# Kernel optimization log

Measured on AMD Instinct MI355X. Metric: run time of the kernel, lower is better.

The kernel has to match this reference:

```python
import jax, jax.numpy as jnp
import numpy as np

F_, H_, W_ = 6, 16, 28          # latent video grid (frames, height, width)
DIM, NH = 1536, 12
HD = DIM // NH                   # 128
L = F_ * H_ * W_                 # 2688 tokens
EPS = 1e-6
BLOCK = 3 * H_ * W_              # block_causal_size = 3*frame_height*frame_width


def setup_inputs() -> dict:
    key = jax.random.key(0)
    ks = jax.random.split(key, 8)
    def lin(k):
        return jax.random.normal(k, (DIM, DIM), jnp.float32) * 0.02
    x = jax.random.normal(ks[0], (1, L, DIM), jnp.float32)
    # RoPE freqs: unit-modulus complex numbers stored as [...,(re,im)]
    ang = jax.random.uniform(ks[1], (1024, HD // 2), jnp.float32, -np.pi, np.pi)
    freqs = jnp.stack([jnp.cos(ang), jnp.sin(ang)], axis=-1)  # [1024, 64, 2]
    return {
        'x': x,
        'seq_lens': jnp.array([L], jnp.int32),
        'grid_sizes': jnp.array([[F_, H_, W_]], jnp.int32),
        'freqs': freqs,
        'Wq': lin(ks[2]), 'bq': jnp.zeros((DIM,), jnp.float32),
        'Wk': lin(ks[3]), 'bk': jnp.zeros((DIM,), jnp.float32),
        'Wv': lin(ks[4]), 'bv': jnp.zeros((DIM,), jnp.float32),
        'Wo': lin(ks[5]), 'bo': jnp.zeros((DIM,), jnp.float32),
        'gq': jnp.ones((DIM,), jnp.float32),
        'gk': jnp.ones((DIM,), jnp.float32),
    }


def _rmsnorm(x, g):
    # WanRMSNorm: x * rsqrt(mean(x^2) + eps) * weight
    return x * jax.lax.rsqrt(jnp.mean(x * x, axis=-1, keepdims=True) + EPS) * g


def _rope_apply(x, F, H, W, freqs, start_frame=0):
    # x: [B, L, n, d]; freqs: [1024, d//2, 2] (re, im). Per-axis split [c0, c3, c3].
    B, Lx, n, d = x.shape
    c = d // 2
    c3 = c // 3
    c0 = c - 2 * c3
    f0 = freqs[start_frame:start_frame + F, :c0]      # [F, c0, 2]
    f1 = freqs[:H, c0:c0 + c3]                        # [H, c3, 2]
    f2 = freqs[:W, c0 + c3:]                          # [W, c3, 2]
    ff = jnp.concatenate([
        jnp.broadcast_to(f0[:, None, None], (F, H, W, c0, 2)),
        jnp.broadcast_to(f1[None, :, None], (F, H, W, c3, 2)),
        jnp.broadcast_to(f2[None, None, :], (F, H, W, c3, 2)),
    ], axis=3).reshape(Lx, 1, c, 2)                   # [L, 1, c, 2]
    xr = x.reshape(B, Lx, n, c, 2)
    xre, xim = xr[..., 0], xr[..., 1]
    fre, fim = ff[None, ..., 0], ff[None, ..., 1]     # broadcast over batch, heads
    ore = xre * fre - xim * fim
    oim = xre * fim + xim * fre
    return jnp.stack([ore, oim], axis=-1).reshape(B, Lx, n, d)


def reference(x, seq_lens, grid_sizes, freqs, Wq, bq, Wk, bk, Wv, bv, Wo, bo, gq, gk):
    b, s = x.shape[:2]
    F = int(grid_sizes[0, 0]); H = int(grid_sizes[0, 1]); W = int(grid_sizes[0, 2])
    q = _rmsnorm(x @ Wq + bq, gq).reshape(b, s, NH, HD)
    k = _rmsnorm(x @ Wk + bk, gk).reshape(b, s, NH, HD)
    v = (x @ Wv + bv).reshape(b, s, NH, HD)
    rq = _rope_apply(q, F, H, W, freqs)
    rk = _rope_apply(k, F, H, W, freqs)
    # block-causal attention: query attends to keys in same-or-earlier 3-frame block
    scores = jnp.einsum('bihd,bjhd->bhij', rq, rk) * (HD ** -0.5)
    blk = jnp.arange(s) // (3 * H * W)
    mask = blk[None, :] <= blk[:, None]               # [s, s]
    scores = jnp.where(mask[None, None], scores, -1e30)
    attn = jax.nn.softmax(scores, axis=-1)
    out = jnp.einsum('bhij,bjhd->bihd', attn, v).reshape(b, s, DIM)
    return out @ Wo + bo
```

## Files before the change

kernel.cpp:

```cpp
#include <hip/hip_runtime.h>

#define L_SEQ 2688
#define DIM   1536
#define NH    12
#define HD    128
#define BLK_TOK 1344
#define HW_   448
#define W_    28

typedef unsigned short u16;
typedef unsigned int   u32;
typedef __attribute__((ext_vector_type(4))) float f32x4;
typedef __attribute__((ext_vector_type(8))) short s16x8;

__device__ __forceinline__ u16 f2b(float f) {
    u32 u = __builtin_bit_cast(u32, f);
    return (u16)((u + 0x7FFFu + ((u >> 16) & 1u)) >> 16);
}
__device__ __forceinline__ float b2f(u16 b) {
    return __builtin_bit_cast(float, (u32)b << 16);
}

__global__ __launch_bounds__(256) void k_cvt_x(const float* __restrict__ x,
                                               u16* __restrict__ xb, int n4) {
    int i = blockIdx.x * 256 + threadIdx.x;
    int stride = gridDim.x * 256;
    for (; i < n4; i += stride) {
        float4 v = ((const float4*)x)[i];
        ushort4 o;
        o.x = f2b(v.x); o.y = f2b(v.y); o.z = f2b(v.z); o.w = f2b(v.w);
        ((ushort4*)xb)[i] = o;
    }
}

__global__ __launch_bounds__(256) void k_trans_w(const float* __restrict__ w0,
                                                 const float* __restrict__ w1,
                                                 const float* __restrict__ w2,
                                                 const float* __restrict__ w3,
                                                 u16* __restrict__ wt_all) {
    const float* w = blockIdx.z == 0 ? w0 : blockIdx.z == 1 ? w1 : blockIdx.z == 2 ? w2 : w3;
    u16* wt = wt_all + (size_t)blockIdx.z * DIM * DIM;
    __shared__ float t[64][65];
    const int k0 = blockIdx.y * 64, n0 = blockIdx.x * 64;
    const int c = threadIdx.x & 63, rg = threadIdx.x >> 6;
#pragma unroll
    for (int it = 0; it < 16; ++it) {
        int r = rg * 16 + it;
        t[r][c] = w[(size_t)(k0 + r) * DIM + n0 + c];
    }
    __syncthreads();
#pragma unroll
    for (int it = 0; it < 16; ++it) {
        int r = rg * 16 + it;
        wt[(size_t)(n0 + r) * DIM + k0 + c] = f2b(t[c][r]);
    }
}

template<int OUTF>
__global__ __launch_bounds__(256, 2) void k_gemm(const u16* __restrict__ A,
                                                 const u16* __restrict__ Bt_all,
                                                 const float* __restrict__ b0,
                                                 const float* __restrict__ b1,
                                                 const float* __restrict__ b2,
                                                 void* __restrict__ out_all) {
    const int z = blockIdx.z;
    const u16* Bt = Bt_all + (size_t)z * DIM * DIM;
    const float* bias = z == 0 ? b0 : z == 1 ? b1 : b2;

    __shared__ u16 lA[128 * 32];
    __shared__ u16 lB[128 * 32];
    const int tid = threadIdx.x, lane = tid & 63, wid = tid >> 6;
    const int wm = wid >> 1, wn = wid & 1;
    const int bm = blockIdx.y, bn = blockIdx.x;
    const int lr = lane & 15, lg = lane >> 4;

    f32x4 acc[4][4] = {};

    for (int kt = 0; kt < DIM / 32; ++kt) {
#pragma unroll
        for (int i = 0; i < 2; ++i) {
            int s = wid * 128 + i * 64 + lane;
            int row = s >> 2, c16 = s & 3;
            const u16* ga = A + (size_t)(bm * 128 + row) * DIM + kt * 32 + c16 * 8;
            __builtin_amdgcn_global_load_lds(
                (const __attribute__((address_space(1))) u32*)ga,
                (__attribute__((address_space(3))) u32*)&lA[(wid * 128 + i * 64) * 8],
                16, 0, 0);
            const u16* gb = Bt + (size_t)(bn * 128 + row) * DIM + kt * 32 + c16 * 8;
            __builtin_amdgcn_global_load_lds(
                (const __attribute__((address_space(1))) u32*)gb,
                (__attribute__((address_space(3))) u32*)&lB[(wid * 128 + i * 64) * 8],
                16, 0, 0);
        }
        __syncthreads();
        s16x8 af[4], bf[4];
#pragma unroll
        for (int m = 0; m < 4; ++m)
            af[m] = *(const s16x8*)&lA[(wm * 64 + m * 16 + lr) * 32 + lg * 8];
#pragma unroll
        for (int n = 0; n < 4; ++n)
            bf[n] = *(const s16x8*)&lB[(wn * 64 + n * 16 + lr) * 32 + lg * 8];
#pragma unroll
        for (int m = 0; m < 4; ++m)
#pragma unroll
            for (int n = 0; n < 4; ++n)
                acc[m][n] = __builtin_amdgcn_mfma_f32_16x16x32_bf16(af[m], bf[n], acc[m][n], 0, 0, 0);
        __syncthreads();
    }
#pragma unroll
    for (int n = 0; n < 4; ++n) {
        int col = bn * 128 + wn * 64 + n * 16 + lr;
        float bv = bias[col];
#pragma unroll
        for (int m = 0; m < 4; ++m) {
            int row0 = bm * 128 + wm * 64 + m * 16 + lg * 4;
#pragma unroll
            for (int r = 0; r < 4; ++r) {
                float v = acc[m][n][r] + bv;
                if (OUTF)
                    ((float*)out_all)[(size_t)(row0 + r) * DIM + col] = v;
                else
                    ((u16*)out_all)[(size_t)z * L_SEQ * DIM + (size_t)(row0 + r) * DIM + col] = f2b(v);
            }
        }
    }
}

__global__ __launch_bounds__(256) void k_norm_rope(const u16* __restrict__ pre_all,
                                                   const float* __restrict__ gq,
                                                   const float* __restrict__ gk,
                                                   const float* __restrict__ freqs,
                                                   u16* __restrict__ qh,
                                                   u16* __restrict__ kh) {
    const int which = blockIdx.y;
    const u16* pre = pre_all + (size_t)which * L_SEQ * DIM;
    const float* g = which ? gk : gq;
    u16* outh = which ? kh : qh;

    const int i = blockIdx.x;
    const int t = threadIdx.x;
    const u32* prow = (const u32*)(pre + (size_t)i * DIM);

    float re[3], im[3];
    float ss = 0.f;
#pragma unroll
    for (int a = 0; a < 3; ++a) {
        u32 p = prow[t + a * 256];
        float x = b2f((u16)(p & 0xFFFFu)), y = b2f((u16)(p >> 16));
        re[a] = x; im[a] = y;
        ss += x * x + y * y;
    }
#pragma unroll
    for (int o = 32; o > 0; o >>= 1) ss += __shfl_down(ss, o, 64);
    __shared__ float sred[4];
    if ((t & 63) == 0) sred[t >> 6] = ss;
    __syncthreads();
    float rms = rsqrtf((sred[0] + sred[1] + sred[2] + sred[3]) * (1.0f / DIM) + 1e-6f);

    const int f = i / HW_;
    const int rem = i - f * HW_;
    const int hp = rem / W_;
    const int wp = rem - hp * W_;
#pragma unroll
    for (int a = 0; a < 3; ++a) {
        int j = t + a * 256;
        int h = j >> 6, pj = j & 63;
        float2 gg = ((const float2*)g)[j];
        float x = re[a] * rms * gg.x;
        float y = im[a] * rms * gg.y;
        int ridx = pj < 22 ? f : (pj < 43 ? hp : wp);
        float2 cs = ((const float2*)freqs)[ridx * 64 + pj];
        float ore = x * cs.x - y * cs.y;
        float oim = x * cs.y + y * cs.x;
        u32 o = (u32)f2b(ore) | ((u32)f2b(oim) << 16);
        ((u32*)outh)[(size_t)h * (L_SEQ * 64) + (size_t)i * 64 + pj] = o;
    }
}

__global__ __launch_bounds__(256) void k_vtrans(const u16* __restrict__ vpre,
                                                u16* __restrict__ vt) {
    const int i0 = blockIdx.x * 64, d0 = blockIdx.y * 64, h = blockIdx.z;
    __shared__ u16 t[64][68];
    const int c = threadIdx.x & 63, rg = threadIdx.x >> 6;
#pragma unroll
    for (int it = 0; it < 16; ++it) {
        int r = rg * 16 + it;
        t[r][c] = vpre[(size_t)(i0 + r) * DIM + h * HD + d0 + c];
    }
    __syncthreads();
#pragma unroll
    for (int it = 0; it < 16; ++it) {
        int r = rg * 16 + it;
        vt[(size_t)h * (HD * L_SEQ) + (size_t)(d0 + r) * L_SEQ + i0 + c] = t[c][r];
    }
}

__global__ __launch_bounds__(256, 2) void k_attn(const u16* __restrict__ qh,
                                                 const u16* __restrict__ kh,
                                                 const u16* __restrict__ vt,
                                                 u16* __restrict__ ob,
                                                 float* __restrict__ Opart,
                                                 float* __restrict__ mlp) {
    __shared__ u16 lK[2][64 * 128];
    __shared__ u16 lV[2][128 * 64];
    __shared__ u16 lP[64 * 64];

    const int flat = blockIdx.x;
    const int xcd = flat & 7, idx = flat >> 3;
    const int work = (xcd < 4) ? (xcd * 95 + idx) : (380 + (xcd - 4) * 94 + idx);
    const int head = work / 63;
    const int bx = work - head * 63;
    int qt, kv0, mode;
    if (bx < 21)      { qt = bx;      kv0 = 0;  mode = 0; }
    else if (bx < 42) { qt = bx;      kv0 = 0;  mode = 1; }
    else              { qt = bx - 21; kv0 = 21; mode = 2; }

    const int tid = threadIdx.x, lane = tid & 63, wid = tid >> 6;
    const int lr = lane & 15, lg = lane >> 4;
    const size_t hOff = (size_t)head * ((size_t)L_SEQ * HD);
    const u16* Kh = kh + hOff;
    const u16* Vh = vt + hOff;
    const int qrow0 = qt * 64 + wid * 16;

    s16x8 aq[4];
#pragma unroll
    for (int kk = 0; kk < 4; ++kk)
        aq[kk] = *(const s16x8*)&qh[hOff + (size_t)(qrow0 + lr) * HD + kk * 32 + lg * 8];

    const u16* kap[4]; const u16* vap[4];
    int ldsb[4];
#pragma unroll
    for (int i = 0; i < 4; ++i) {
        int jrow = wid * 16 + i * 4 + lg;
        kap[i] = Kh + (size_t)(kv0 * 64 + jrow) * HD + 8 * ((lane & 15) ^ (i * 4 + lg));
        int drow = wid * 32 + i * 8 + (lane >> 3);
        vap[i] = Vh + (size_t)drow * L_SEQ + kv0 * 64 + 8 * ((lane & 7) ^ ((lane >> 3) & 7));
        ldsb[i] = wid * 4096 + i * 1024;
    }
#define STAGE(T, BUF)                                                              \
    {                                                                              \
        _Pragma("unroll")                                                          \
        for (int i = 0; i < 4; ++i)                                                \
            __builtin_amdgcn_global_load_lds(                                      \
                (const __attribute__((address_space(1))) u32*)(kap[i] + (size_t)(T) * 8192), \
                (__attribute__((address_space(3))) u32*)((char*)&lK[BUF][0] + ldsb[i]), 16, 0, 0); \
        _Pragma("unroll")                                                          \
        for (int i = 0; i < 4; ++i)                                                \
            __builtin_amdgcn_global_load_lds(                                      \
                (const __attribute__((address_space(1))) u32*)(vap[i] + (T) * 64), \
                (__attribute__((address_space(3))) u32*)((char*)&lV[BUF][0] + ldsb[i]), 16, 0, 0); \
    }

    f32x4 acc[8] = {};
    float mrun = -1e30f, lrun = 0.f;
    const float sc2 = 0.12751739646917983f;
    const int prow = wid * 16 + lr;
    const int pswz = (lr & 7) << 4;

    STAGE(0, 0);
    for (int t = 0; t < 21; ++t) {
        __syncthreads();
        if (t < 20) STAGE(t + 1, (t + 1) & 1);
        const u16* bK = lK[t & 1];
        const u16* bV = lV[t & 1];

        f32x4 sv[4] = {};
        __builtin_amdgcn_s_setprio(1);
#pragma unroll
        for (int n = 0; n < 4; ++n) {
#pragma unroll
            for (int kk = 0; kk < 4; ++kk) {
                int off = (16 * n + lr) * 256 + ((64 * kk + 16 * lg) ^ (lr << 4));
                s16x8 kf = *(const s16x8*)((const char*)bK + off);
                sv[n] = __builtin_amdgcn_mfma_f32_16x16x32_bf16(kf, aq[kk], sv[n], 0, 0, 0);
            }
        }
        __builtin_amdgcn_s_setprio(0);

        float mx = sv[0][0];
#pragma unroll
        for (int n = 0; n < 4; ++n) {
            mx = fmaxf(mx, fmaxf(fmaxf(sv[n][0], sv[n][1]), fmaxf(sv[n][2], sv[n][3])));
        }
        mx = fmaxf(mx, __shfl_xor(mx, 16, 64));
        mx = fmaxf(mx, __shfl_xor(mx, 32, 64));
        mx *= sc2;
        const int resc = (mx - mrun) > 11.5f;
        const float mm = resc ? mx : mrun;
        const float fac = resc ? __builtin_amdgcn_exp2f(mrun - mm) : 1.0f;
        mrun = mm;
        float p[4][4];
        float sum = 0.f;
#pragma unroll
        for (int n = 0; n < 4; ++n)
#pragma unroll
            for (int r = 0; r < 4; ++r) {
                float pv = __builtin_amdgcn_exp2f(sv[n][r] * sc2 - mm);
                p[n][r] = pv;
                sum += pv;
            }
        sum += __shfl_xor(sum, 16, 64);
        sum += __shfl_xor(sum, 32, 64);
        lrun = lrun * fac + sum;
        if (__any(resc)) {
#pragma unroll
            for (int r = 0; r < 4; ++r) {
                float fr = __shfl(fac, 4 * lg + r, 64);
#pragma unroll
                for (int nd = 0; nd < 8; ++nd) acc[nd][r] *= fr;
            }
        }

#pragma unroll
        for (int n = 0; n < 4; ++n) {
            u32 lo = (u32)f2b(p[n][0]) | ((u32)f2b(p[n][1]) << 16);
            u32 hi = (u32)f2b(p[n][2]) | ((u32)f2b(p[n][3]) << 16);
            uint2 wpk; wpk.x = lo; wpk.y = hi;
            int addr = prow * 128 + ((32 * n + 8 * lg) ^ pswz);
            *(uint2*)((char*)lP + addr) = wpk;
        }

        __builtin_amdgcn_s_setprio(1);
#pragma unroll
        for (int kk2 = 0; kk2 < 2; ++kk2) {
            int pa_off = prow * 128 + ((64 * kk2 + 16 * lg) ^ pswz);
            s16x8 pa = *(const s16x8*)((const char*)lP + pa_off);
#pragma unroll
            for (int nd = 0; nd < 8; ++nd) {
                int va = (16 * nd + lr) * 128 + ((64 * kk2 + 16 * lg) ^ ((lr & 7) << 4));
                s16x8 bvv = *(const s16x8*)((const char*)bV + va);
                acc[nd] = __builtin_amdgcn_mfma_f32_16x16x32_bf16(pa, bvv, acc[nd], 0, 0, 0);
            }
        }
        __builtin_amdgcn_s_setprio(0);
    }

    if (mode == 0) {
#pragma unroll
        for (int r = 0; r < 4; ++r) {
            float invl = 1.0f / __shfl(lrun, 4 * lg + r, 64);
            int row = qrow0 + 4 * lg + r;
#pragma unroll
            for (int nd = 0; nd < 8; ++nd)
                ob[(size_t)row * DIM + head * HD + nd * 16 + lr] = f2b(acc[nd][r] * invl);
        }
    } else {
        const int pair = (head * 21 + (qt - 21)) * 2 + (mode - 1);
        float* Op = Opart + (size_t)pair * (64 * 128);
#pragma unroll
        for (int r = 0; r < 4; ++r) {
            int rowl = wid * 16 + 4 * lg + r;
#pragma unroll
            for (int nd = 0; nd < 8; ++nd)
                Op[rowl * 128 + nd * 16 + lr] = acc[nd][r];
        }
        if (lg == 0) {
            float2 ml; ml.x = mrun; ml.y = lrun;
            ((float2*)mlp)[(size_t)pair * 64 + wid * 16 + lr] = ml;
        }
    }
#undef STAGE
}

__global__ __launch_bounds__(256) void k_merge(const float* __restrict__ Opart,
                                               const float* __restrict__ mlp,
                                               u16* __restrict__ ob) {
    const int b = blockIdx.x;
    const int qt2 = b % 21, head = b / 21;
    const int pair = head * 21 + qt2;
    const float* O0 = Opart + (size_t)pair * 2 * 8192;
    const float* O1 = O0 + 8192;
    const int tid = threadIdx.x;
    const int row = tid >> 2, cs = (tid & 3) * 32;
    float2 a = ((const float2*)mlp)[(size_t)pair * 2 * 64 + row];
    float2 c = ((const float2*)mlp)[(size_t)(pair * 2 + 1) * 64 + row];
    float M = fmaxf(a.x, c.x);
    float w0 = exp2f(a.x - M), w1 = exp2f(c.x - M);
    float inv = 1.0f / (w0 * a.y + w1 * c.y);
    w0 *= inv; w1 *= inv;
    const int rowg = BLK_TOK + qt2 * 64 + row;
    u32* orow = (u32*)(ob + (size_t)rowg * DIM + head * HD + cs);
    const float4* p0 = (const float4*)(O0 + row * 128 + cs);
    const float4* p1 = (const float4*)(O1 + row * 128 + cs);
#pragma unroll
    for (int u = 0; u < 8; ++u) {
        float4 x0 = p0[u], x1 = p1[u];
        float o0 = x0.x * w0 + x1.x * w1;
        float o1 = x0.y * w0 + x1.y * w1;
        float o2 = x0.z * w0 + x1.z * w1;
        float o3 = x0.w * w0 + x1.w * w1;
        orow[u * 2]     = (u32)f2b(o0) | ((u32)f2b(o1) << 16);
        orow[u * 2 + 1] = (u32)f2b(o2) | ((u32)f2b(o3) << 16);
    }
}

extern "C" void kernel_launch(void* const* d_in, const int* in_sizes, int n_in,
                              void* d_out, int out_size, void* d_ws, size_t ws_size,
                              hipStream_t stream) {
    const float* x     = (const float*)d_in[0];
    const float* freqs = (const float*)d_in[3];
    const float* Wq    = (const float*)d_in[4];
    const float* bq    = (const float*)d_in[5];
    const float* Wk    = (const float*)d_in[6];
    const float* bk    = (const float*)d_in[7];
    const float* Wv    = (const float*)d_in[8];
    const float* bv    = (const float*)d_in[9];
    const float* Wo    = (const float*)d_in[10];
    const float* bo    = (const float*)d_in[11];
    const float* gq    = (const float*)d_in[12];
    const float* gk    = (const float*)d_in[13];

    const size_t LD = (size_t)L_SEQ * DIM;
    u16* wt_all  = (u16*)d_ws;
    u16* xb      = wt_all + (size_t)4 * DIM * DIM;
    u16* pre_all = xb + LD;
    u16* qh      = pre_all + 3 * LD;
    u16* kh2     = qh + LD;
    u16* vt      = kh2 + LD;
    u16* ob      = vt + LD;
    float* Opart = (float*)pre_all;
    float* mlp   = Opart + (size_t)12 * 21 * 2 * 64 * 128;

    k_cvt_x<<<2016, 256, 0, stream>>>(x, xb, (int)(LD / 4));
    k_trans_w<<<dim3(24, 24, 4), 256, 0, stream>>>(Wq, Wk, Wv, Wo, wt_all);
    k_gemm<0><<<dim3(12, 21, 3), 256, 0, stream>>>(xb, wt_all, bq, bk, bv, pre_all);
    k_norm_rope<<<dim3(L_SEQ, 2), 256, 0, stream>>>(pre_all, gq, gk, freqs, qh, kh2);
    k_vtrans<<<dim3(42, 2, NH), 256, 0, stream>>>(pre_all + 2 * LD, vt);
    k_attn<<<dim3(756), 256, 0, stream>>>(qh, kh2, vt, ob, Opart, mlp);
    k_merge<<<dim3(252), 256, 0, stream>>>(Opart, mlp, ob);
    k_gemm<1><<<dim3(12, 21, 1), 256, 0, stream>>>(ob, wt_all + (size_t)3 * DIM * DIM, bo, bo, bo, d_out);
}
```

Before: 188.8 us.

## Use two waves with 32 query rows each in attention, reusing K/V fragments

The attention kernel now runs 128 threads (2 waves), each wave handling 32 query rows as two 16-row groups. Each K and V fragment read from LDS feeds two MFMAs, halving LDS read traffic per MFMA. Staging is reworked so 2 waves load the full K/V tiles, and P is packed with the hardware v_cvt_pk_bf16_f32 instruction instead of manual rounding. The cost is more registers per wave and fewer waves per block, which reduces latency hiding and occupancy.

```diff
diff --git a/kernel.cpp b/kernel.cpp
--- a/kernel.cpp
+++ b/kernel.cpp
@@ -19,6 +19,11 @@
 }
 __device__ __forceinline__ float b2f(u16 b) {
     return __builtin_bit_cast(float, (u32)b << 16);
+}
+__device__ __forceinline__ u32 cvt_pk_bf16(float lo, float hi) {
+    u32 r;
+    asm("v_cvt_pk_bf16_f32 %0, %1, %2" : "=v"(r) : "v"(lo), "v"(hi));
+    return r;
 }
 
 __global__ __launch_bounds__(256) void k_cvt_x(const float* __restrict__ x,
@@ -195,7 +200,7 @@
     }
 }
 
-__global__ __launch_bounds__(256, 2) void k_attn(const u16* __restrict__ qh,
+__global__ __launch_bounds__(128, 2) void k_attn(const u16* __restrict__ qh,
                                                  const u16* __restrict__ kh,
                                                  const u16* __restrict__ vt,
                                                  u16* __restrict__ ob,
@@ -215,46 +220,52 @@
     else if (bx < 42) { qt = bx;      kv0 = 0;  mode = 1; }
     else              { qt = bx - 21; kv0 = 21; mode = 2; }
 
-    const int tid = threadIdx.x, lane = tid & 63, wid = tid >> 6;
+    const int tid = threadIdx.x, lane = tid & 63, w = tid >> 6;
     const int lr = lane & 15, lg = lane >> 4;
+    const int dl = lane >> 3, cv = lane & 7;
     const size_t hOff = (size_t)head * ((size_t)L_SEQ * HD);
     const u16* Kh = kh + hOff;
     const u16* Vh = vt + hOff;
-    const int qrow0 = qt * 64 + wid * 16;
-
-    s16x8 aq[4];
-#pragma unroll
-    for (int kk = 0; kk < 4; ++kk)
-        aq[kk] = *(const s16x8*)&qh[hOff + (size_t)(qrow0 + lr) * HD + kk * 32 + lg * 8];
-
-    const u16* kap[4]; const u16* vap[4];
-    int ldsb[4];
-#pragma unroll
-    for (int i = 0; i < 4; ++i) {
-        int jrow = wid * 16 + i * 4 + lg;
-        kap[i] = Kh + (size_t)(kv0 * 64 + jrow) * HD + 8 * ((lane & 15) ^ (i * 4 + lg));
-        int drow = wid * 32 + i * 8 + (lane >> 3);
-        vap[i] = Vh + (size_t)drow * L_SEQ + kv0 * 64 + 8 * ((lane & 7) ^ ((lane >> 3) & 7));
-        ldsb[i] = wid * 4096 + i * 1024;
-    }
-#define STAGE(T, BUF)                                                              \
-    {                                                                              \
-        _Pragma("unroll")                                                          \
-        for (int i = 0; i < 4; ++i)                                                \
-            __builtin_amdgcn_global_load_lds(                                      \
-                (const __attribute__((address_space(1))) u32*)(kap[i] + (size_t)(T) * 8192), \
-                (__attribute__((address_space(3))) u32*)((char*)&lK[BUF][0] + ldsb[i]), 16, 0, 0); \
-        _Pragma("unroll")                                                          \
-        for (int i = 0; i < 4; ++i)                                                \
-            __builtin_amdgcn_global_load_lds(                                      \
-                (const __attribute__((address_space(1))) u32*)(vap[i] + (T) * 64), \
-                (__attribute__((address_space(3))) u32*)((char*)&lV[BUF][0] + ldsb[i]), 16, 0, 0); \
-    }
-
-    f32x4 acc[8] = {};
-    float mrun = -1e30f, lrun = 0.f;
+    const int qrow0 = qt * 64 + w * 32;
+
+    s16x8 aq[2][4];
+#pragma unroll
+    for (int g = 0; g < 2; ++g)
+#pragma unroll
+        for (int kk = 0; kk < 4; ++kk)
+            aq[g][kk] = *(const s16x8*)&qh[hOff + (size_t)(qrow0 + 16 * g + lr) * HD + kk * 32 + lg * 8];
+
+    const int voffK0 = lg * HD + 8 * (lr ^ ((w << 2) | lg));
+    const int voffK1 = lg * HD + 8 * (lr ^ (((2 + w) << 2) | lg));
+    const int voffV  = dl * L_SEQ + 8 * (cv ^ dl);
+
+#define STAGE(T, BUF)                                                               \
+    {                                                                               \
+        _Pragma("unroll")                                                           \
+        for (int i = 0; i < 8; ++i) {                                               \
+            const u16* src = Kh + (size_t)(kv0 + (T)) * 8192 + (2 * i + w) * 512 +  \
+                             ((i & 1) ? voffK1 : voffK0);                           \
+            __builtin_amdgcn_global_load_lds(                                       \
+                (const __attribute__((address_space(1))) u32*)src,                  \
+                (__attribute__((address_space(3))) u32*)&lK[BUF][(2 * i + w) * 512],\
+                16, 0, 0);                                                          \
+        }                                                                           \
+        _Pragma("unroll")                                                           \
+        for (int i = 0; i < 8; ++i) {                                               \
+            const u16* src = Vh + (size_t)(kv0 + (T)) * 64 +                        \
+                             (size_t)(2 * i + w) * 8 * L_SEQ + voffV;               \
+            __builtin_amdgcn_global_load_lds(                                       \
+                (const __attribute__((address_space(1))) u32*)src,                  \
+                (__attribute__((address_space(3))) u32*)&lV[BUF][(2 * i + w) * 512],\
+                16, 0, 0);                                                          \
+        }                                                                           \
+    }
+
+    f32x4 acc[2][8] = {};
+    float mrun[2], lrun[2];
+#pragma unroll
+    for (int g = 0; g < 2; ++g) { mrun[g] = -1e30f; lrun[g] = 0.f; }
     const float sc2 = 0.12751739646917983f;
-    const int prow = wid * 16 + lr;
     const int pswz = (lr & 7) << 4;
 
     STAGE(0, 0);
@@ -264,7 +275,7 @@
         const u16* bK = lK[t & 1];
         const u16* bV = lV[t & 1];
 
-        f32x4 sv[4] = {};
+        f32x4 sv[2][4] = {};
         __builtin_amdgcn_s_setprio(1);
 #pragma unroll
         for (int n = 0; n < 4; ++n) {
@@ -272,91 +283,112 @@
             for (int kk = 0; kk < 4; ++kk) {
                 int off = (16 * n + lr) * 256 + ((64 * kk + 16 * lg) ^ (lr << 4));
                 s16x8 kf = *(const s16x8*)((const char*)bK + off);
-                sv[n] = __builtin_amdgcn_mfma_f32_16x16x32_bf16(kf, aq[kk], sv[n], 0, 0, 0);
+                sv[0][n] = __builtin_amdgcn_mfma_f32_16x16x32_bf16(kf, aq[0][kk], sv[0][n], 0, 0, 0);
+                sv[1][n] = __builtin_amdgcn_mfma_f32_16x16x32_bf16(kf, aq[1][kk], sv[1][n], 0, 0, 0);
             }
         }
         __builtin_amdgcn_s_setprio(0);
 
-        float mx = sv[0][0];
-#pragma unroll
-        for (int n = 0; n < 4; ++n) {
-            mx = fmaxf(mx, fmaxf(fmaxf(sv[n][0], sv[n][1]), fmaxf(sv[n][2], sv[n][3])));
-        }
-        mx = fmaxf(mx, __shfl_xor(mx, 16, 64));
-        mx = fmaxf(mx, __shfl_xor(mx, 32, 64));
-        mx *= sc2;
-        const int resc = (mx - mrun) > 11.5f;
-        const float mm = resc ? mx : mrun;
-        const float fac = resc ? __builtin_amdgcn_exp2f(mrun - mm) : 1.0f;
-        mrun = mm;
-        float p[4][4];
-        float sum = 0.f;
-#pragma unroll
-        for (int n = 0; n < 4; ++n)
+        float fac[2];
+        int anyr = 0;
+#pragma unroll
+        for (int g = 0; g < 2; ++g) {
+            float mx = sv[g][0][0];
+#pragma unroll
+            for (int n = 0; n < 4; ++n)
+                mx = fmaxf(mx, fmaxf(fmaxf(sv[g][n][0], sv[g][n][1]),
+                                     fmaxf(sv[g][n][2], sv[g][n][3])));
+            mx = fmaxf(mx, __shfl_xor(mx, 16, 64));
+            mx = fmaxf(mx, __shfl_xor(mx, 32, 64));
+            mx *= sc2;
+            const int resc = (mx - mrun[g]) > 11.5f;
+            const float mm = resc ? mx : mrun[g];
+            fac[g] = resc ? __builtin_amdgcn_exp2f(mrun[g] - mm) : 1.0f;
+            mrun[g] = mm;
+            anyr |= resc;
+            float sum = 0.f;
+#pragma unroll
+            for (int n = 0; n < 4; ++n)
+#pragma unroll
+                for (int r = 0; r < 4; ++r) {
+                    float pv = __builtin_amdgcn_exp2f(sv[g][n][r] * sc2 - mm);
+                    sv[g][n][r] = pv;
+                    sum += pv;
+                }
+            sum += __shfl_xor(sum, 16, 64);
+            sum += __shfl_xor(sum, 32, 64);
+            lrun[g] = lrun[g] * fac[g] + sum;
+        }
+        if (__any(anyr)) {
+#pragma unroll
+            for (int g = 0; g < 2; ++g)
+#pragma unroll
+                for (int r = 0; r < 4; ++r) {
+                    float fr = __shfl(fac[g], 4 * lg + r, 64);
+#pragma unroll
+                    for (int nd = 0; nd < 8; ++nd) acc[g][nd][r] *= fr;
+                }
+        }
+
+#pragma unroll
+        for (int g = 0; g < 2; ++g) {
+            int row = w * 32 + 16 * g + lr;
+#pragma unroll
+            for (int n = 0; n < 4; ++n) {
+                uint2 wpk;
+                wpk.x = cvt_pk_bf16(sv[g][n][0], sv[g][n][1]);
+                wpk.y = cvt_pk_bf16(sv[g][n][2], sv[g][n][3]);
+                int addr = row * 128 + ((32 * n + 8 * lg) ^ pswz);
+                *(uint2*)((char*)lP + addr) = wpk;
+            }
+        }
+
+        __builtin_amdgcn_s_setprio(1);
+#pragma unroll
+        for (int kk2 = 0; kk2 < 2; ++kk2) {
+            int cb = (64 * kk2 + 16 * lg);
+            s16x8 pa0 = *(const s16x8*)((const char*)lP + (w * 32 + lr) * 128 + (cb ^ pswz));
+            s16x8 pa1 = *(const s16x8*)((const char*)lP + (w * 32 + 16 + lr) * 128 + (cb ^ pswz));
+#pragma unroll
+            for (int nd = 0; nd < 8; ++nd) {
+                int va = (16 * nd + lr) * 128 + (cb ^ pswz);
+                s16x8 bvv = *(const s16x8*)((const char*)bV + va);
+                acc[0][nd] = __builtin_amdgcn_mfma_f32_16x16x32_bf16(pa0, bvv, acc[0][nd], 0, 0, 0);
+                acc[1][nd] = __builtin_amdgcn_mfma_f32_16x16x32_bf16(pa1, bvv, acc[1][nd], 0, 0, 0);
+            }
+        }
+        __builtin_amdgcn_s_setprio(0);
+    }
+
+    if (mode == 0) {
+#pragma unroll
+        for (int g = 0; g < 2; ++g)
 #pragma unroll
             for (int r = 0; r < 4; ++r) {
-                float pv = __builtin_amdgcn_exp2f(sv[n][r] * sc2 - mm);
-                p[n][r] = pv;
-                sum += pv;
-            }
-        sum += __shfl_xor(sum, 16, 64);
-        sum += __shfl_xor(sum, 32, 64);
-        lrun = lrun * fac + sum;
-        if (__any(resc)) {
-#pragma unroll
-            for (int r = 0; r < 4; ++r) {
-                float fr = __shfl(fac, 4 * lg + r, 64);
-#pragma unroll
-                for (int nd = 0; nd < 8; ++nd) acc[nd][r] *= fr;
-            }
-        }
-
-#pragma unroll
-        for (int n = 0; n < 4; ++n) {
-            u32 lo = (u32)f2b(p[n][0]) | ((u32)f2b(p[n][1]) << 16);
-            u32 hi = (u32)f2b(p[n][2]) | ((u32)f2b(p[n][3]) << 16);
-            uint2 wpk; wpk.x = lo; wpk.y = hi;
-            int addr = prow * 128 + ((32 * n + 8 * lg) ^ pswz);
-            *(uint2*)((char*)lP + addr) = wpk;
-        }
-
-        __builtin_amdgcn_s_setprio(1);
-#pragma unroll
-        for (int kk2 = 0; kk2 < 2; ++kk2) {
-            int pa_off = prow * 128 + ((64 * kk2 + 16 * lg) ^ pswz);
-            s16x8 pa = *(const s16x8*)((const char*)lP + pa_off);
-#pragma unroll
-            for (int nd = 0; nd < 8; ++nd) {
-                int va = (16 * nd + lr) * 128 + ((64 * kk2 + 16 * lg) ^ ((lr & 7) << 4));
-                s16x8 bvv = *(const s16x8*)((const char*)bV + va);
-                acc[nd] = __builtin_amdgcn_mfma_f32_16x16x32_bf16(pa, bvv, acc[nd], 0, 0, 0);
-            }
-        }
-        __builtin_amdgcn_s_setprio(0);
-    }
-
-    if (mode == 0) {
-#pragma unroll
-        for (int r = 0; r < 4; ++r) {
-            float invl = 1.0f / __shfl(lrun, 4 * lg + r, 64);
-            int row = qrow0 + 4 * lg + r;
-#pragma unroll
-            for (int nd = 0; nd < 8; ++nd)
-                ob[(size_t)row * DIM + head * HD + nd * 16 + lr] = f2b(acc[nd][r] * invl);
-        }
+                float invl = 1.0f / __shfl(lrun[g], 4 * lg + r, 64);
+                int row = qrow0 + 16 * g + 4 * lg + r;
+#pragma unroll
+                for (int nd = 0; nd < 8; ++nd)
+                    ob[(size_t)row * DIM + head * HD + nd * 16 + lr] = f2b(acc[g][nd][r] * invl);
+            }
     } else {
         const int pair = (head * 21 + (qt - 21)) * 2 + (mode - 1);
         float* Op = Opart + (size_t)pair * (64 * 128);
 #pragma unroll
-        for (int r = 0; r < 4; ++r) {
-            int rowl = wid * 16 + 4 * lg + r;
-#pragma unroll
-            for (int nd = 0; nd < 8; ++nd)
-                Op[rowl * 128 + nd * 16 + lr] = acc[nd][r];
-        }
+        for (int g = 0; g < 2; ++g)
+#pragma unroll
+            for (int r = 0; r < 4; ++r) {
+                int rowl = w * 32 + 16 * g + 4 * lg + r;
+#pragma unroll
+                for (int nd = 0; nd < 8; ++nd)
+                    Op[rowl * 128 + nd * 16 + lr] = acc[g][nd][r];
+            }
         if (lg == 0) {
-            float2 ml; ml.x = mrun; ml.y = lrun;
-            ((float2*)mlp)[(size_t)pair * 64 + wid * 16 + lr] = ml;
+#pragma unroll
+            for (int g = 0; g < 2; ++g) {
+                float2 ml; ml.x = mrun[g]; ml.y = lrun[g];
+                ((float2*)mlp)[(size_t)pair * 64 + w * 32 + 16 * g + lr] = ml;
+            }
         }
     }
 #undef STAGE
@@ -426,7 +458,7 @@
     k_gemm<0><<<dim3(12, 21, 3), 256, 0, stream>>>(xb, wt_all, bq, bk, bv, pre_all);
     k_norm_rope<<<dim3(L_SEQ, 2), 256, 0, stream>>>(pre_all, gq, gk, freqs, qh, kh2);
     k_vtrans<<<dim3(42, 2, NH), 256, 0, stream>>>(pre_all + 2 * LD, vt);
-    k_attn<<<dim3(756), 256, 0, stream>>>(qh, kh2, vt, ob, Opart, mlp);
+    k_attn<<<dim3(756), 128, 0, stream>>>(qh, kh2, vt, ob, Opart, mlp);
     k_merge<<<dim3(252), 256, 0, stream>>>(Opart, mlp, ob);
     k_gemm<1><<<dim3(12, 21, 1), 256, 0, stream>>>(ob, wt_all + (size_t)3 * DIM * DIM, bo, bo, bo, d_out);
 }
```

New measurement: 204.3 us. 8.2% more time.

## Load V fragments directly from global into registers, drop V LDS staging

Applied to the files above, without the earlier changes.

Removes the shared-memory double buffer for V. Each wave now loads its V MFMA operands straight from global memory into registers every iteration, issued after the QK MFMAs so the loads overlap the softmax. The freed LDS lets occupancy rise to 3 blocks per CU, and the bf16 packing of P uses the hardware packed-convert instruction. The cost is that every wave reads the full V tile redundantly from global/L2 with no prefetch, and 16 extra vector registers per thread add register pressure at the higher occupancy target.

```diff
diff --git a/kernel.cpp b/kernel.cpp
--- a/kernel.cpp
+++ b/kernel.cpp
@@ -19,6 +19,11 @@
 }
 __device__ __forceinline__ float b2f(u16 b) {
     return __builtin_bit_cast(float, (u32)b << 16);
+}
+__device__ __forceinline__ u32 cvt_pk_bf16(float lo, float hi) {
+    u32 r;
+    asm("v_cvt_pk_bf16_f32 %0, %1, %2" : "=v"(r) : "v"(lo), "v"(hi));
+    return r;
 }
 
 __global__ __launch_bounds__(256) void k_cvt_x(const float* __restrict__ x,
@@ -195,14 +200,13 @@
     }
 }
 
-__global__ __launch_bounds__(256, 2) void k_attn(const u16* __restrict__ qh,
+__global__ __launch_bounds__(256, 3) void k_attn(const u16* __restrict__ qh,
                                                  const u16* __restrict__ kh,
                                                  const u16* __restrict__ vt,
                                                  u16* __restrict__ ob,
                                                  float* __restrict__ Opart,
                                                  float* __restrict__ mlp) {
     __shared__ u16 lK[2][64 * 128];
-    __shared__ u16 lV[2][128 * 64];
     __shared__ u16 lP[64 * 64];
 
     const int flat = blockIdx.x;
@@ -227,14 +231,12 @@
     for (int kk = 0; kk < 4; ++kk)
         aq[kk] = *(const s16x8*)&qh[hOff + (size_t)(qrow0 + lr) * HD + kk * 32 + lg * 8];
 
-    const u16* kap[4]; const u16* vap[4];
+    const u16* kap[4];
     int ldsb[4];
 #pragma unroll
     for (int i = 0; i < 4; ++i) {
         int jrow = wid * 16 + i * 4 + lg;
         kap[i] = Kh + (size_t)(kv0 * 64 + jrow) * HD + 8 * ((lane & 15) ^ (i * 4 + lg));
-        int drow = wid * 32 + i * 8 + (lane >> 3);
-        vap[i] = Vh + (size_t)drow * L_SEQ + kv0 * 64 + 8 * ((lane & 7) ^ ((lane >> 3) & 7));
         ldsb[i] = wid * 4096 + i * 1024;
     }
 #define STAGE(T, BUF)                                                              \
@@ -244,12 +246,9 @@
             __builtin_amdgcn_global_load_lds(                                      \
                 (const __attribute__((address_space(1))) u32*)(kap[i] + (size_t)(T) * 8192), \
                 (__attribute__((address_space(3))) u32*)((char*)&lK[BUF][0] + ldsb[i]), 16, 0, 0); \
-        _Pragma("unroll")                                                          \
-        for (int i = 0; i < 4; ++i)                                                \
-            __builtin_amdgcn_global_load_lds(                                      \
-                (const __attribute__((address_space(1))) u32*)(vap[i] + (T) * 64), \
-                (__attribute__((address_space(3))) u32*)((char*)&lV[BUF][0] + ldsb[i]), 16, 0, 0); \
-    }
+    }
+
+    const u16* Vp = Vh + (size_t)lr * L_SEQ + kv0 * 64 + lg * 8;
 
     f32x4 acc[8] = {};
     float mrun = -1e30f, lrun = 0.f;
@@ -262,7 +261,7 @@
         __syncthreads();
         if (t < 20) STAGE(t + 1, (t + 1) & 1);
         const u16* bK = lK[t & 1];
-        const u16* bV = lV[t & 1];
+        const u16* Vt = Vp + t * 64;
 
         f32x4 sv[4] = {};
         __builtin_amdgcn_s_setprio(1);
@@ -276,6 +275,13 @@
             }
         }
         __builtin_amdgcn_s_setprio(0);
+
+        s16x8 vf[16];
+#pragma unroll
+        for (int nd = 0; nd < 8; ++nd)
+#pragma unroll
+            for (int kk2 = 0; kk2 < 2; ++kk2)
+                vf[nd * 2 + kk2] = *(const s16x8*)(Vt + (size_t)(16 * nd) * L_SEQ + kk2 * 32);
 
         float mx = sv[0][0];
 #pragma unroll
@@ -313,9 +319,9 @@
 
 #pragma unroll
         for (int n = 0; n < 4; ++n) {
-            u32 lo = (u32)f2b(p[n][0]) | ((u32)f2b(p[n][1]) << 16);
-            u32 hi = (u32)f2b(p[n][2]) | ((u32)f2b(p[n][3]) << 16);
-            uint2 wpk; wpk.x = lo; wpk.y = hi;
+            uint2 wpk;
+            wpk.x = cvt_pk_bf16(p[n][0], p[n][1]);
+            wpk.y = cvt_pk_bf16(p[n][2], p[n][3]);
             int addr = prow * 128 + ((32 * n + 8 * lg) ^ pswz);
             *(uint2*)((char*)lP + addr) = wpk;
         }
@@ -326,11 +332,8 @@
             int pa_off = prow * 128 + ((64 * kk2 + 16 * lg) ^ pswz);
             s16x8 pa = *(const s16x8*)((const char*)lP + pa_off);
 #pragma unroll
-            for (int nd = 0; nd < 8; ++nd) {
-                int va = (16 * nd + lr) * 128 + ((64 * kk2 + 16 * lg) ^ ((lr & 7) << 4));
-                s16x8 bvv = *(const s16x8*)((const char*)bV + va);
-                acc[nd] = __builtin_amdgcn_mfma_f32_16x16x32_bf16(pa, bvv, acc[nd], 0, 0, 0);
-            }
+            for (int nd = 0; nd < 8; ++nd)
+                acc[nd] = __builtin_amdgcn_mfma_f32_16x16x32_bf16(pa, vf[nd * 2 + kk2], acc[nd], 0, 0, 0);
         }
         __builtin_amdgcn_s_setprio(0);
     }
```

Measured after the change: 246.0 us. 1.3x slower.
